# Kernel optimization log

Measured on AMD Instinct MI355X. Metric: run time of the kernel, lower is better.

The kernel has to match this reference:

```python
import jax, jax.numpy as jnp
import numpy as np

B, LH, HF = 65536, 128, 32
VC_MIN = 0.0


def _theta_init():
    # Deterministic parameter init, matching the torch constructor defaults.
    def spinv(x):
        return float(np.log(np.exp(max(x, 1e-4)) - 1.0 + 1e-6))
    vals = [
        0.0,                                  # alpha_raw: log(0.5/(1-0.5))
        float(np.log(np.exp(1.0) - 1.0 + 1e-6)),   # c_raw  (c_init=1.0)
        float(np.log(np.exp(0.1) - 1.0 + 1e-6)),   # kappa_raw (kappa_init=0.1)
        float(np.log(np.exp(0.15) - 1.0 + 1e-6)),  # vc_raw (vc_eff=0.15)
        -6.0,   # log_qx
        -6.0,   # log_qu
        -5.0,   # log_r
        0.0,    # log_q_scale
        -6.0,   # log_p0_xx
        -4.0,   # log_p0_uu
        spinv(0.1),   # a1_raw
        spinv(0.05),  # d1_raw
        spinv(0.5),   # d2_raw
        spinv(0.5),   # d3_raw
        0.0,    # b1
        0.0,    # b2
        0.1,    # beta
        float(np.arctanh(0.9)),  # rho_m_raw
        -4.0,   # log_qm
        -4.0,   # log_p0_mm
    ]
    return np.asarray(vals, dtype=np.float32)


def setup_inputs() -> dict:
    key = jax.random.key(0)
    k1, k2, k3, k4, k5 = jax.random.split(key, 5)
    return {
        "v_hist": jax.random.normal(k1, (B, LH), dtype=jnp.float32),
        "dt_hist": 0.01 + 0.1 * jax.random.uniform(k2, (B, LH), dtype=jnp.float32),
        "x_obs_hist": jax.random.normal(k3, (B, LH), dtype=jnp.float32),
        "v_fut": jax.random.normal(k4, (B, HF), dtype=jnp.float32),
        "dt_fut": 0.01 + 0.1 * jax.random.uniform(k5, (B, HF), dtype=jnp.float32),
        "theta": jnp.asarray(_theta_init()),
    }


def _forward(v_hist, dt_hist, x_obs_hist, v_fut, dt_fut, theta):
    sp = jax.nn.softplus
    alpha = jax.nn.sigmoid(theta[0])
    c = sp(theta[1]); kappa = sp(theta[2]); vc = sp(theta[3]) + VC_MIN
    qx = jnp.exp(theta[4]); qu = jnp.exp(theta[5]); R = jnp.exp(theta[6])
    qs = jnp.exp(theta[7]); p0xx = jnp.exp(theta[8]); p0uu = jnp.exp(theta[9])
    a1 = sp(theta[10]); d1 = sp(theta[11]); d2 = sp(theta[12]); d3 = sp(theta[13])
    b1 = theta[14]; b2 = theta[15]; beta = theta[16]
    rho_m = jnp.tanh(theta[17]); qm = jnp.exp(theta[18]); p0mm = jnp.exp(theta[19])

    Bn, Lh = v_hist.shape
    dtype = v_hist.dtype
    eye = jnp.eye(3, dtype=dtype)

    def predict(s, P, v, dv, dt):
        x, u, m = s[:, 0], s[:, 1], s[:, 2]
        rho = jnp.exp(-alpha * dt)
        forcing = jax.nn.relu(v * v - vc * vc)
        cl = (-a1 * u + b1 * v + b2 * dv
              - d1 * u * u - d2 * u * jnp.abs(v) - d3 * u * jnp.abs(u))
        x_p = x + u * dt
        u_p = rho * u - kappa * x * dt + c * forcing * dt + cl * dt + beta * m
        m_p = rho_m * m
        s_p = jnp.stack([x_p, u_p, m_p], axis=1)
        z = jnp.zeros_like(dt); o = jnp.ones_like(dt)
        Fm = jnp.stack([
            jnp.stack([o, dt, z], axis=1),
            jnp.stack([-kappa * dt, rho, beta * o], axis=1),
            jnp.stack([z, z, rho_m * o], axis=1)], axis=1)  # [B,3,3]
        qdiag = jnp.stack([qs * qx * dt, qs * qu * dt, qm * o], axis=1)  # [B,3]
        P_p = jnp.einsum('bij,bjk,blk->bil', Fm, P, Fm) + qdiag[:, :, None] * eye
        return s_p, P_p

    def update(s, P, y):
        innov = y - s[:, 0]
        S = P[:, 0, 0] + R
        K = P[:, :, 0] / S[:, None]            # [B,3]
        s_u = s + K * innov[:, None]
        IKH = eye - K[:, :, None] * eye[0]     # I - K H, H = [1,0,0]
        P_u = (jnp.einsum('bij,bjk,blk->bil', IKH, P, IKH)
               + R * (K[:, :, None] * K[:, None, :]))
        return s_u, P_u

    s0 = jnp.zeros((Bn, 3), dtype).at[:, 0].set(x_obs_hist[:, 0])
    P0 = jnp.broadcast_to(jnp.diag(jnp.stack([p0xx, p0uu, p0mm])).astype(dtype),
                          (Bn, 3, 3))

    # History steps k = 1 .. Lh-1 (scan over time axis, [T, B] layout)
    v_h = v_hist[:, :Lh - 1].T
    dv_h = jnp.concatenate(
        [jnp.zeros((1, Bn), dtype), (v_hist[:, 1:Lh - 1] - v_hist[:, :Lh - 2]).T], axis=0)
    dt_h = jnp.maximum(dt_hist[:, 1:], 1e-6).T
    y_h = x_obs_hist[:, 1:].T

    def hist_step(carry, inp):
        s, P = carry
        v, dv, dt, y = inp
        s, P = predict(s, P, v, dv, dt)
        s, P = update(s, P, y)
        return (s, P), None

    (s, P), _ = jax.lax.scan(hist_step, (s0, P0), (v_h, dv_h, dt_h, y_h))

    # Future rollout (predict only)
    v_f = v_fut.T
    dv_f = (v_fut - jnp.concatenate([v_hist[:, -1:], v_fut[:, :-1]], axis=1)).T
    dt_f = jnp.maximum(dt_fut, 1e-6).T

    def fut_step(carry, inp):
        s, P = carry
        v, dv, dt = inp
        s, P = predict(s, P, v, dv, dt)
        return (s, P), (s[:, 0], P[:, 0, 0], s[:, 1])

    _, (x_preds, x_vars, u_ests) = jax.lax.scan(fut_step, (s, P), (v_f, dv_f, dt_f))
    return x_preds.T, x_vars.T, u_ests.T  # each [B, Hf]


def reference(v_hist, dt_hist, x_obs_hist, v_fut, dt_fut, theta):
    return _forward(v_hist, dt_hist, x_obs_hist, v_fut, dt_fut, theta)
```

## Files before the change

### kernel.cpp

```cpp
#include <hip/hip_runtime.h>
#include <math.h>

#define BATCH 65536
#define LHIST 128
#define HFUT  32
#define CH    16

__device__ __forceinline__ float softplusf(float x) {
    return fmaxf(x, 0.0f) + log1pf(expf(-fabsf(x)));
}

__global__ __launch_bounds__(256, 1) void kalman_fwd(
    const float* __restrict__ v_hist,
    const float* __restrict__ dt_hist,
    const float* __restrict__ x_obs,
    const float* __restrict__ v_fut,
    const float* __restrict__ dt_fut,
    const float* __restrict__ theta,
    float* __restrict__ out)
{
    const int b = blockIdx.x * blockDim.x + threadIdx.x;

    const float alpha = 1.0f / (1.0f + expf(-theta[0]));
    const float c     = softplusf(theta[1]);
    const float kappa = softplusf(theta[2]);
    const float vc    = softplusf(theta[3]);
    const float qx    = expf(theta[4]);
    const float qu    = expf(theta[5]);
    const float Rn    = expf(theta[6]);
    const float qs    = expf(theta[7]);
    const float p0xx  = expf(theta[8]);
    const float p0uu  = expf(theta[9]);
    const float a1    = softplusf(theta[10]);
    const float d1    = softplusf(theta[11]);
    const float d2    = softplusf(theta[12]);
    const float d3    = softplusf(theta[13]);
    const float b1    = theta[14];
    const float b2    = theta[15];
    const float beta  = theta[16];
    const float rho_m = tanhf(theta[17]);
    const float qm    = expf(theta[18]);
    const float p0mm  = expf(theta[19]);
    const float vc2   = vc * vc;
    const float qxs   = qs * qx;
    const float qus   = qs * qu;
    const float rm2   = rho_m * rho_m;
    const float nal2e = -alpha * 1.44269504088896340736f;

    float sx = 0.0f, su = 0.0f, sm = 0.0f;
    float p00 = p0xx, p01 = 0.0f, p02 = 0.0f, p11 = p0uu, p12 = 0.0f, p22 = p0mm;

    auto predict = [&](float v, float dv, float dt_raw) {
        float dt  = fmaxf(dt_raw, 1e-6f);
        float rho = __builtin_amdgcn_exp2f(nal2e * dt);
        float forcing = fmaxf(v * v - vc2, 0.0f);
        float cl = -a1 * su + b1 * v + b2 * dv
                 - d1 * su * su - d2 * su * fabsf(v) - d3 * su * fabsf(su);
        float kdt = kappa * dt;
        float x_p = sx + su * dt;
        float u_p = rho * su - kdt * sx + c * forcing * dt + cl * dt + beta * sm;
        float m_p = rho_m * sm;
        float f0 = p00 + dt * p01;
        float f1 = p01 + dt * p11;
        float f2 = p02 + dt * p12;
        float g0 = -kdt * p00 + rho * p01 + beta * p02;
        float g1 = -kdt * p01 + rho * p11 + beta * p12;
        float g2 = -kdt * p02 + rho * p12 + beta * p22;
        float n00 = f0 + dt * f1 + qxs * dt;
        float n01 = -kdt * f0 + rho * f1 + beta * f2;
        float n02 = rho_m * f2;
        float n11 = -kdt * g0 + rho * g1 + beta * g2 + qus * dt;
        float n12 = rho_m * g2;
        float n22 = rm2 * p22 + qm;
        sx = x_p; su = u_p; sm = m_p;
        p00 = n00; p01 = n01; p02 = n02; p11 = n11; p12 = n12; p22 = n22;
    };

    auto update = [&](float y) {
        float innov = y - sx;
        float S    = p00 + Rn;
        float Sinv = __builtin_amdgcn_rcpf(S);
        float K0 = p00 * Sinv, K1 = p01 * Sinv, K2 = p02 * Sinv;
        sx += K0 * innov; su += K1 * innov; sm += K2 * innov;
        float a = 1.0f - K0;
        float n00 = a * a * p00 + Rn * K0 * K0;
        float n01 = a * (p01 - K1 * p00) + Rn * K0 * K1;
        float n02 = a * (p02 - K2 * p00) + Rn * K0 * K2;
        float n11 = S * K1 * K1 - 2.0f * K1 * p01 + p11;
        float n12 = S * K1 * K2 - K2 * p01 - K1 * p02 + p12;
        float n22 = S * K2 * K2 - 2.0f * K2 * p02 + p22;
        p00 = n00; p01 = n01; p02 = n02; p11 = n11; p12 = n12; p22 = n22;
    };

    const float4* v4  = (const float4*)(v_hist  + (size_t)b * LHIST);
    const float4* d4  = (const float4*)(dt_hist + (size_t)b * LHIST);
    const float4* y4  = (const float4*)(x_obs   + (size_t)b * LHIST);

    float cv[CH], cd[CH], cy[CH];
    float nv[CH], nd[CH], ny[CH];

    auto load_chunk = [&](float (&vv)[CH], float (&dd)[CH], float (&yy)[CH], int k) {
        float4* V = (float4*)vv; float4* D = (float4*)dd; float4* Y = (float4*)yy;
        #pragma unroll
        for (int i = 0; i < CH / 4; ++i) {
            V[i] = v4[(CH / 4) * k + i];
            D[i] = d4[(CH / 4) * k + i];
            Y[i] = y4[(CH / 4) * k + i];
        }
    };

    float vf[HFUT], df[HFUT];

    load_chunk(cv, cd, cy, 0);
    load_chunk(nv, nd, ny, 1);
    __builtin_amdgcn_sched_barrier(0);

    sx = cy[0];
    predict(cv[0], 0.0f, cd[1]); update(cy[1]);
    #pragma unroll
    for (int i = 1; i < CH - 1; ++i) {
        predict(cv[i], cv[i] - cv[i - 1], cd[i + 1]); update(cy[i + 1]);
    }
    float v_bridge  = cv[CH - 1];
    float dv_bridge = cv[CH - 1] - cv[CH - 2];

    #pragma unroll 1
    for (int k = 1; k < LHIST / CH - 1; ++k) {
        #pragma unroll
        for (int i = 0; i < CH; ++i) { cv[i] = nv[i]; cd[i] = nd[i]; cy[i] = ny[i]; }
        load_chunk(nv, nd, ny, k + 1);
        __builtin_amdgcn_sched_barrier(0);
        predict(v_bridge, dv_bridge, cd[0]); update(cy[0]);
        predict(cv[0], cv[0] - v_bridge, cd[1]); update(cy[1]);
        #pragma unroll
        for (int i = 1; i < CH - 1; ++i) {
            predict(cv[i], cv[i] - cv[i - 1], cd[i + 1]); update(cy[i + 1]);
        }
        v_bridge  = cv[CH - 1];
        dv_bridge = cv[CH - 1] - cv[CH - 2];
    }

    {
        #pragma unroll
        for (int i = 0; i < CH; ++i) { cv[i] = nv[i]; cd[i] = nd[i]; cy[i] = ny[i]; }
        {
            const float4* vf4 = (const float4*)(v_fut  + (size_t)b * HFUT);
            const float4* df4 = (const float4*)(dt_fut + (size_t)b * HFUT);
            float4* VF = (float4*)vf; float4* DF = (float4*)df;
            #pragma unroll
            for (int i = 0; i < HFUT / 4; ++i) { VF[i] = vf4[i]; DF[i] = df4[i]; }
        }
        __builtin_amdgcn_sched_barrier(0);
        predict(v_bridge, dv_bridge, cd[0]); update(cy[0]);
        predict(cv[0], cv[0] - v_bridge, cd[1]); update(cy[1]);
        #pragma unroll
        for (int i = 1; i < CH - 1; ++i) {
            predict(cv[i], cv[i] - cv[i - 1], cd[i + 1]); update(cy[i + 1]);
        }
        v_bridge = cv[CH - 1];
    }

    float oxp[HFUT], oxv[HFUT], oue[HFUT];
    float vp = v_bridge;
    #pragma unroll
    for (int j = 0; j < HFUT; ++j) {
        predict(vf[j], vf[j] - vp, df[j]);
        vp = vf[j];
        oxp[j] = sx; oxv[j] = p00; oue[j] = su;
    }

    float4* xp = (float4*)(out + (size_t)b * HFUT);
    float4* xv = (float4*)(out + (size_t)BATCH * HFUT + (size_t)b * HFUT);
    float4* ue = (float4*)(out + 2 * (size_t)BATCH * HFUT + (size_t)b * HFUT);
    float4* OXP = (float4*)oxp; float4* OXV = (float4*)oxv; float4* OUE = (float4*)oue;
    #pragma unroll
    for (int i = 0; i < HFUT / 4; ++i) {
        xp[i] = OXP[i]; xv[i] = OXV[i]; ue[i] = OUE[i];
    }
}

extern "C" void kernel_launch(void* const* d_in, const int* in_sizes, int n_in,
                              void* d_out, int out_size, void* d_ws, size_t ws_size,
                              hipStream_t stream) {
    const float* v_hist  = (const float*)d_in[0];
    const float* dt_hist = (const float*)d_in[1];
    const float* x_obs   = (const float*)d_in[2];
    const float* v_fut   = (const float*)d_in[3];
    const float* dt_fut  = (const float*)d_in[4];
    const float* theta   = (const float*)d_in[5];
    float* out = (float*)d_out;

    dim3 grid(BATCH / 256), block(256);
    hipLaunchKernelGGL(kalman_fwd, grid, block, 0, stream,
                       v_hist, dt_hist, x_obs, v_fut, dt_fut, theta, out);
}
```

Measured before the change: 170.0 us.

## Stage history chunks through LDS via async global_load_lds double buffering

Replaces the register-based prefetch of the next history chunk with asynchronous global-to-LDS loads (global_load_lds, 16 bytes per lane) into a per-wave double buffer, then reads each chunk from LDS into registers before processing. The aim is to cut register pressure from holding two chunks in VGPRs and to overlap the global loads with the serial Kalman recurrence. The future inputs are staged the same way. This adds 128KB of LDS per block and relies on hand-written vmcnt/lgkmcnt waits, so any miscount in the wait values risks races.

```diff
diff --git a/kernel.cpp b/kernel.cpp
--- a/kernel.cpp
+++ b/kernel.cpp
@@ -8,6 +8,12 @@
 
 __device__ __forceinline__ float softplusf(float x) {
     return fmaxf(x, 0.0f) + log1pf(expf(-fabsf(x)));
+}
+
+__device__ __forceinline__ void gload16(const float* g, float* l) {
+    __builtin_amdgcn_global_load_lds(
+        (const __attribute__((address_space(1))) void*)g,
+        (__attribute__((address_space(3))) void*)l, 16, 0, 0);
 }
 
 __global__ __launch_bounds__(256, 1) void kalman_fwd(
@@ -19,7 +25,12 @@
     const float* __restrict__ theta,
     float* __restrict__ out)
 {
-    const int b = blockIdx.x * blockDim.x + threadIdx.x;
+    const int b    = blockIdx.x * blockDim.x + threadIdx.x;
+    const int lane = threadIdx.x & 63;
+    const int wid  = threadIdx.x >> 6;
+
+    __shared__ __align__(16) float lds[32768];
+    const int wbase = wid * 8192;
 
     const float alpha = 1.0f / (1.0f + expf(-theta[0]));
     const float c     = softplusf(theta[1]);
@@ -92,44 +103,57 @@
         p00 = n00; p01 = n01; p02 = n02; p11 = n11; p12 = n12; p22 = n22;
     };
 
-    const float4* v4  = (const float4*)(v_hist  + (size_t)b * LHIST);
-    const float4* d4  = (const float4*)(dt_hist + (size_t)b * LHIST);
-    const float4* y4  = (const float4*)(x_obs   + (size_t)b * LHIST);
+    const float* vrow = v_hist  + (size_t)b * LHIST;
+    const float* drow = dt_hist + (size_t)b * LHIST;
+    const float* yrow = x_obs   + (size_t)b * LHIST;
+
+    auto stage_hist = [&](int k, int buf) {
+        float* base = &lds[wbase + buf * 4096];
+        #pragma unroll
+        for (int j = 0; j < 4; ++j) {
+            gload16(vrow + k * CH + 4 * j, base +        j * 256);
+            gload16(drow + k * CH + 4 * j, base + 1024 + j * 256);
+            gload16(yrow + k * CH + 4 * j, base + 2048 + j * 256);
+        }
+    };
 
     float cv[CH], cd[CH], cy[CH];
-    float nv[CH], nd[CH], ny[CH];
-
-    auto load_chunk = [&](float (&vv)[CH], float (&dd)[CH], float (&yy)[CH], int k) {
-        float4* V = (float4*)vv; float4* D = (float4*)dd; float4* Y = (float4*)yy;
-        #pragma unroll
-        for (int i = 0; i < CH / 4; ++i) {
-            V[i] = v4[(CH / 4) * k + i];
-            D[i] = d4[(CH / 4) * k + i];
-            Y[i] = y4[(CH / 4) * k + i];
-        }
-    };
-
-    float vf[HFUT], df[HFUT];
-
-    load_chunk(cv, cd, cy, 0);
-    load_chunk(nv, nd, ny, 1);
+    auto read_chunk = [&](int buf) {
+        const float* base = &lds[wbase + buf * 4096 + lane * 4];
+        #pragma unroll
+        for (int j = 0; j < 4; ++j) {
+            *(float4*)&cv[4 * j] = *(const float4*)(base +        j * 256);
+            *(float4*)&cd[4 * j] = *(const float4*)(base + 1024 + j * 256);
+            *(float4*)&cy[4 * j] = *(const float4*)(base + 2048 + j * 256);
+        }
+    };
+
+    asm volatile("s_waitcnt vmcnt(0)" ::: "memory");
     __builtin_amdgcn_sched_barrier(0);
 
+    float v_bridge = 0.0f, dv_bridge = 0.0f;
+
+    stage_hist(0, 0);
+    stage_hist(1, 1);
+    asm volatile("s_waitcnt vmcnt(12)" ::: "memory");
+    __builtin_amdgcn_sched_barrier(0);
+    read_chunk(0);
     sx = cy[0];
     predict(cv[0], 0.0f, cd[1]); update(cy[1]);
     #pragma unroll
     for (int i = 1; i < CH - 1; ++i) {
         predict(cv[i], cv[i] - cv[i - 1], cd[i + 1]); update(cy[i + 1]);
     }
-    float v_bridge  = cv[CH - 1];
-    float dv_bridge = cv[CH - 1] - cv[CH - 2];
+    v_bridge  = cv[CH - 1];
+    dv_bridge = cv[CH - 1] - cv[CH - 2];
 
     #pragma unroll 1
-    for (int k = 1; k < LHIST / CH - 1; ++k) {
-        #pragma unroll
-        for (int i = 0; i < CH; ++i) { cv[i] = nv[i]; cd[i] = nd[i]; cy[i] = ny[i]; }
-        load_chunk(nv, nd, ny, k + 1);
+    for (int k = 1; k < 7; ++k) {
+        asm volatile("s_waitcnt lgkmcnt(0)" ::: "memory");
+        stage_hist(k + 1, (k + 1) & 1);
+        asm volatile("s_waitcnt vmcnt(12)" ::: "memory");
         __builtin_amdgcn_sched_barrier(0);
+        read_chunk(k & 1);
         predict(v_bridge, dv_bridge, cd[0]); update(cy[0]);
         predict(cv[0], cv[0] - v_bridge, cd[1]); update(cy[1]);
         #pragma unroll
@@ -141,16 +165,17 @@
     }
 
     {
-        #pragma unroll
-        for (int i = 0; i < CH; ++i) { cv[i] = nv[i]; cd[i] = nd[i]; cy[i] = ny[i]; }
-        {
-            const float4* vf4 = (const float4*)(v_fut  + (size_t)b * HFUT);
-            const float4* df4 = (const float4*)(dt_fut + (size_t)b * HFUT);
-            float4* VF = (float4*)vf; float4* DF = (float4*)df;
-            #pragma unroll
-            for (int i = 0; i < HFUT / 4; ++i) { VF[i] = vf4[i]; DF[i] = df4[i]; }
-        }
+        asm volatile("s_waitcnt lgkmcnt(0)" ::: "memory");
+        const float* vfrow = v_fut  + (size_t)b * HFUT;
+        const float* dfrow = dt_fut + (size_t)b * HFUT;
+        float* base = &lds[wbase];
+        #pragma unroll
+        for (int j = 0; j < 8; ++j) gload16(vfrow + 4 * j, base +        j * 256);
+        #pragma unroll
+        for (int j = 0; j < 8; ++j) gload16(dfrow + 4 * j, base + 2048 + j * 256);
+        asm volatile("s_waitcnt vmcnt(16)" ::: "memory");
         __builtin_amdgcn_sched_barrier(0);
+        read_chunk(1);
         predict(v_bridge, dv_bridge, cd[0]); update(cy[0]);
         predict(cv[0], cv[0] - v_bridge, cd[1]); update(cy[1]);
         #pragma unroll
@@ -158,6 +183,18 @@
             predict(cv[i], cv[i] - cv[i - 1], cd[i + 1]); update(cy[i + 1]);
         }
         v_bridge = cv[CH - 1];
+    }
+
+    asm volatile("s_waitcnt vmcnt(0)" ::: "memory");
+    __builtin_amdgcn_sched_barrier(0);
+    float vf[HFUT], df[HFUT];
+    {
+        const float* base = &lds[wbase + lane * 4];
+        #pragma unroll
+        for (int j = 0; j < 8; ++j) {
+            *(float4*)&vf[4 * j] = *(const float4*)(base +        j * 256);
+            *(float4*)&df[4 * j] = *(const float4*)(base + 2048 + j * 256);
+        }
     }
 
     float oxp[HFUT], oxv[HFUT], oue[HFUT];
```

Result: slower. 180.4 us (+6.2%).

## Stage history loads through padded LDS tiles for coalesced global access

Applied to the files above, without the earlier changes.

Each wave now loads 64 rows of history data cooperatively: four lanes cover one contiguous 64-byte row segment, which is written into a padded per-wave LDS tile. Each lane then reads its own row back from LDS in float4 groups for the sequential filter. This replaces the per-thread row-strided float4 loads, which touched a different 512-byte-strided row in every lane, and removes the register double-buffer copies. In exchange it adds LDS traffic and relies on wave-synchronous execution within a single LDS buffer, with no explicit barrier.

```diff
diff --git a/kernel.cpp b/kernel.cpp
--- a/kernel.cpp
+++ b/kernel.cpp
@@ -5,6 +5,9 @@
 #define LHIST 128
 #define HFUT  32
 #define CH    16
+#define PITCH 20
+#define TILE  (64 * PITCH)
+#define BUFSZ (3 * TILE)
 
 __device__ __forceinline__ float softplusf(float x) {
     return fmaxf(x, 0.0f) + log1pf(expf(-fabsf(x)));
@@ -19,7 +22,14 @@
     const float* __restrict__ theta,
     float* __restrict__ out)
 {
-    const int b = blockIdx.x * blockDim.x + threadIdx.x;
+    const int tid  = threadIdx.x;
+    const int b    = blockIdx.x * 256 + tid;
+    const int lane = tid & 63;
+    const int wid  = tid >> 6;
+    const int b0   = blockIdx.x * 256 + wid * 64;
+
+    __shared__ __align__(16) float lds[4 * BUFSZ];
+    float* wl = &lds[wid * BUFSZ];
 
     const float alpha = 1.0f / (1.0f + expf(-theta[0]));
     const float c     = softplusf(theta[1]);
@@ -92,76 +102,99 @@
         p00 = n00; p01 = n01; p02 = n02; p11 = n11; p12 = n12; p22 = n22;
     };
 
-    const float4* v4  = (const float4*)(v_hist  + (size_t)b * LHIST);
-    const float4* d4  = (const float4*)(dt_hist + (size_t)b * LHIST);
-    const float4* y4  = (const float4*)(x_obs   + (size_t)b * LHIST);
-
-    float cv[CH], cd[CH], cy[CH];
-    float nv[CH], nd[CH], ny[CH];
-
-    auto load_chunk = [&](float (&vv)[CH], float (&dd)[CH], float (&yy)[CH], int k) {
-        float4* V = (float4*)vv; float4* D = (float4*)dd; float4* Y = (float4*)yy;
-        #pragma unroll
-        for (int i = 0; i < CH / 4; ++i) {
-            V[i] = v4[(CH / 4) * k + i];
-            D[i] = d4[(CH / 4) * k + i];
-            Y[i] = y4[(CH / 4) * k + i];
-        }
-    };
+    const int    srow = b0 + (lane >> 2);
+    const int    scol = (lane & 3) * 4;
+    const float* gv = v_hist  + (size_t)srow * LHIST + scol;
+    const float* gd = dt_hist + (size_t)srow * LHIST + scol;
+    const float* gy = x_obs   + (size_t)srow * LHIST + scol;
+    float*       lw = wl + (lane >> 2) * PITCH + scol;
+    const float* lr = wl + lane * PITCH;
+
+    float4 sv[4], sd[4], sy[4];
+
+    auto issue_loads = [&](int k) {
+        #pragma unroll
+        for (int i = 0; i < 4; ++i) {
+            sv[i] = *(const float4*)(gv + (size_t)i * 16 * LHIST + k * CH);
+            sd[i] = *(const float4*)(gd + (size_t)i * 16 * LHIST + k * CH);
+            sy[i] = *(const float4*)(gy + (size_t)i * 16 * LHIST + k * CH);
+        }
+    };
+    auto write_stage = [&]() {
+        #pragma unroll
+        for (int i = 0; i < 4; ++i) {
+            *(float4*)(lw + 0 * TILE + i * 16 * PITCH) = sv[i];
+            *(float4*)(lw + 1 * TILE + i * 16 * PITCH) = sd[i];
+            *(float4*)(lw + 2 * TILE + i * 16 * PITCH) = sy[i];
+        }
+    };
+
+    float vp1 = 0.0f, vp2 = 0.0f;
+
+    auto do_group = [&](int g) {
+        float4 v4 = *(const float4*)(lr + 0 * TILE + g * 4);
+        float4 d4 = *(const float4*)(lr + 1 * TILE + g * 4);
+        float4 y4 = *(const float4*)(lr + 2 * TILE + g * 4);
+        const float* vv = (const float*)&v4;
+        const float* dd = (const float*)&d4;
+        const float* yy = (const float*)&y4;
+        #pragma unroll
+        for (int m = 0; m < 4; ++m) {
+            float vcur = vv[m];
+            predict(vp1, vp1 - vp2, dd[m]);
+            update(yy[m]);
+            vp2 = vp1; vp1 = vcur;
+        }
+    };
+
+    issue_loads(0);
+    write_stage();
+    issue_loads(1);
+    __builtin_amdgcn_sched_barrier(0);
+
+    {
+        float4 v4 = *(const float4*)(lr + 0 * TILE);
+        float4 d4 = *(const float4*)(lr + 1 * TILE);
+        float4 y4 = *(const float4*)(lr + 2 * TILE);
+        const float* vv = (const float*)&v4;
+        const float* dd = (const float*)&d4;
+        const float* yy = (const float*)&y4;
+        sx = yy[0]; vp1 = vv[0]; vp2 = vv[0];
+        #pragma unroll
+        for (int m = 1; m < 4; ++m) {
+            float vcur = vv[m];
+            predict(vp1, vp1 - vp2, dd[m]);
+            update(yy[m]);
+            vp2 = vp1; vp1 = vcur;
+        }
+        #pragma unroll
+        for (int g = 1; g < 4; ++g) do_group(g);
+    }
+
+    #pragma unroll 1
+    for (int k = 1; k < 7; ++k) {
+        write_stage();
+        issue_loads(k + 1);
+        __builtin_amdgcn_sched_barrier(0);
+        #pragma unroll
+        for (int g = 0; g < 4; ++g) do_group(g);
+    }
 
     float vf[HFUT], df[HFUT];
-
-    load_chunk(cv, cd, cy, 0);
-    load_chunk(nv, nd, ny, 1);
-    __builtin_amdgcn_sched_barrier(0);
-
-    sx = cy[0];
-    predict(cv[0], 0.0f, cd[1]); update(cy[1]);
-    #pragma unroll
-    for (int i = 1; i < CH - 1; ++i) {
-        predict(cv[i], cv[i] - cv[i - 1], cd[i + 1]); update(cy[i + 1]);
-    }
-    float v_bridge  = cv[CH - 1];
-    float dv_bridge = cv[CH - 1] - cv[CH - 2];
-
-    #pragma unroll 1
-    for (int k = 1; k < LHIST / CH - 1; ++k) {
-        #pragma unroll
-        for (int i = 0; i < CH; ++i) { cv[i] = nv[i]; cd[i] = nd[i]; cy[i] = ny[i]; }
-        load_chunk(nv, nd, ny, k + 1);
+    {
+        write_stage();
+        const float4* vf4 = (const float4*)(v_fut  + (size_t)b * HFUT);
+        const float4* df4 = (const float4*)(dt_fut + (size_t)b * HFUT);
+        float4* VF = (float4*)vf; float4* DF = (float4*)df;
+        #pragma unroll
+        for (int i = 0; i < HFUT / 4; ++i) { VF[i] = vf4[i]; DF[i] = df4[i]; }
         __builtin_amdgcn_sched_barrier(0);
-        predict(v_bridge, dv_bridge, cd[0]); update(cy[0]);
-        predict(cv[0], cv[0] - v_bridge, cd[1]); update(cy[1]);
-        #pragma unroll
-        for (int i = 1; i < CH - 1; ++i) {
-            predict(cv[i], cv[i] - cv[i - 1], cd[i + 1]); update(cy[i + 1]);
-        }
-        v_bridge  = cv[CH - 1];
-        dv_bridge = cv[CH - 1] - cv[CH - 2];
-    }
-
-    {
-        #pragma unroll
-        for (int i = 0; i < CH; ++i) { cv[i] = nv[i]; cd[i] = nd[i]; cy[i] = ny[i]; }
-        {
-            const float4* vf4 = (const float4*)(v_fut  + (size_t)b * HFUT);
-            const float4* df4 = (const float4*)(dt_fut + (size_t)b * HFUT);
-            float4* VF = (float4*)vf; float4* DF = (float4*)df;
-            #pragma unroll
-            for (int i = 0; i < HFUT / 4; ++i) { VF[i] = vf4[i]; DF[i] = df4[i]; }
-        }
-        __builtin_amdgcn_sched_barrier(0);
-        predict(v_bridge, dv_bridge, cd[0]); update(cy[0]);
-        predict(cv[0], cv[0] - v_bridge, cd[1]); update(cy[1]);
-        #pragma unroll
-        for (int i = 1; i < CH - 1; ++i) {
-            predict(cv[i], cv[i] - cv[i - 1], cd[i + 1]); update(cy[i + 1]);
-        }
-        v_bridge = cv[CH - 1];
+        #pragma unroll
+        for (int g = 0; g < 4; ++g) do_group(g);
     }
 
     float oxp[HFUT], oxv[HFUT], oue[HFUT];
-    float vp = v_bridge;
+    float vp = vp1;
     #pragma unroll
     for (int j = 0; j < HFUT; ++j) {
         predict(vf[j], vf[j] - vp, df[j]);
```

Result: slower. 196.6 us (+15.6%).
